# Kernel tuning notes

Measured on AMD Instinct MI355X. Metric: run time of the kernel, lower is better.

The kernel has to match this reference:

```python
import jax, jax.numpy as jnp
import numpy as np

# alpha clamp limits: balance=False -> [exp(-1/5), exp(-1/25)]
ALPHA_MIN = float(np.exp(-1.0 / 5.0))
ALPHA_MAX = float(np.exp(-1.0 / 25.0))
T_CROP = 100


def setup_inputs() -> dict:
    key = jax.random.key(0)
    k1, k2, k3 = jax.random.split(key, 3)
    B, T, D, H = 128, 1000, 1024, 256
    x = jax.random.normal(k1, (B, T, D), dtype=jnp.float32)
    bound = float(np.sqrt(1.0 / D))
    W = jax.random.uniform(k2, (H, D), minval=-bound, maxval=bound, dtype=jnp.float32)
    alpha = jax.random.uniform(k3, (H,), minval=ALPHA_MIN, maxval=ALPHA_MAX, dtype=jnp.float32)
    return {"x": x, "W": W, "alpha": alpha}


def reference(x, W, alpha):
    # x: [B, T, D], W: [H, D], alpha: [H]
    a = jnp.clip(alpha, ALPHA_MIN, ALPHA_MAX)
    Wx = jnp.einsum('btd,hd->bth', x, W)  # [B, T, H]
    T = Wx.shape[1]
    mask = (jnp.arange(T) >= T_CROP).astype(Wx.dtype)  # [T]
    Wx_t = jnp.moveaxis(Wx, 1, 0)  # [T, B, H]

    def step(carry, inp):
        ut, out = carry
        wx, m = inp
        ut = a * ut + (1.0 - a) * wx
        out = out + m * jax.nn.softmax(ut, axis=-1)
        return (ut, out), None

    B, H = Wx.shape[0], Wx.shape[2]
    init = (jnp.zeros((B, H), Wx.dtype), jnp.zeros((B, H), Wx.dtype))
    (_, out), _ = jax.lax.scan(step, init, (Wx_t, mask))
    return out  # [B, H]
```

## Files before the change

### kernel.cpp

```cpp
#include <hip/hip_runtime.h>
#include <hip/hip_bf16.h>

#define B_    128
#define T_    1000
#define D_    1024
#define H_    256
#define TCROP 100
#define CHUNK 25
#define NCHK  40
#define CSKIP 4
#define NOUTC 36

typedef __attribute__((ext_vector_type(8))) short bfrag8;
typedef __attribute__((ext_vector_type(4))) float f32x4;
typedef unsigned long long ull;

__device__ __forceinline__ float bf2f(unsigned short u) {
    union { unsigned int u; float f; } v; v.u = ((unsigned int)u) << 16;
    return v.f;
}
__device__ __forceinline__ unsigned short f2bf(float f) {
    union { float f; unsigned int u; } v; v.f = f;
    unsigned int u = v.u;
    u += 0x7FFFu + ((u >> 16) & 1u);
    return (unsigned short)(u >> 16);
}
__device__ __forceinline__ unsigned int pack2(float lo, float hi) {
    union { float f; unsigned int u; } a, b; a.f = lo; b.f = hi;
    return __builtin_amdgcn_perm(b.u + 0x8000u, a.u + 0x8000u, 0x07060302u);
}
__device__ __forceinline__ bfrag8 cvt8(float4 f0, float4 f1) {
    union { bfrag8 v; unsigned int u[4]; } r;
    r.u[0] = pack2(f0.x, f0.y);
    r.u[1] = pack2(f0.z, f0.w);
    r.u[2] = pack2(f1.x, f1.y);
    r.u[3] = pack2(f1.z, f1.w);
    return r.v;
}

__global__ __launch_bounds__(256) void wconv_kernel(
        const float* __restrict__ W, unsigned short* __restrict__ Wbf) {
    const int i = (blockIdx.x * 256 + threadIdx.x) * 8;
    float4 f0 = *(const float4*)(W + i);
    float4 f1 = *(const float4*)(W + i + 4);
    *(bfrag8*)(Wbf + i) = cvt8(f0, f1);
}

__global__ __launch_bounds__(512) void gemm_kernel(
        const float* __restrict__ x, const unsigned short* __restrict__ Wbf,
        unsigned short* __restrict__ Wx) {
    __shared__ unsigned short As[128 * 64];
    __shared__ unsigned short Bs[256 * 64];

    const int tid  = threadIdx.x;
    const int lane = tid & 63;
    const int wave = tid >> 6;
    const int wr   = wave >> 2;
    const int wc   = wave & 3;
    const int m0   = blockIdx.x * 128;

    f32x4 acc[4][4];
#pragma unroll
    for (int m = 0; m < 4; ++m)
#pragma unroll
        for (int n = 0; n < 4; ++n) acc[m][n] = (f32x4){0.f, 0.f, 0.f, 0.f};

    const int rr  = lane & 15;
    const int kh  = lane >> 4;
    const int ra0 = tid >> 3;
    const int ja  = tid & 7;
    const int sa  = (ja ^ (ra0 & 7)) * 8;
    const float* ap0 = x + (size_t)(m0 + ra0) * D_ + ja * 8;
    const float* ap1 = ap0 + (size_t)64 * D_;

    for (int it = 0; it < 16; ++it) {
        const int kt = it * 64;
        float4 f00 = *(const float4*)(ap0 + kt);
        float4 f01 = *(const float4*)(ap0 + kt + 4);
        float4 f10 = *(const float4*)(ap1 + kt);
        float4 f11 = *(const float4*)(ap1 + kt + 4);
#pragma unroll
        for (int q = 0; q < 4; ++q) {
            const int li = q * 512 + tid;
            const int r = li >> 3, j = li & 7;
            const int jj = j ^ (r & 7);
            __builtin_amdgcn_global_load_lds(
                (const __attribute__((address_space(1))) void*)
                    (Wbf + (size_t)r * D_ + kt + jj * 8),
                (__attribute__((address_space(3))) void*)&Bs[li * 8], 16, 0, 0);
        }
        *(bfrag8*)&As[ra0 * 64 + sa]        = cvt8(f00, f01);
        *(bfrag8*)&As[(ra0 + 64) * 64 + sa] = cvt8(f10, f11);
        __syncthreads();
#pragma unroll
        for (int kk = 0; kk < 2; ++kk) {
            const int c16 = kk * 4 + kh;
            bfrag8 af[4], bfr[4];
#pragma unroll
            for (int m = 0; m < 4; ++m) {
                const int row = wr * 64 + m * 16 + rr;
                af[m] = *(const bfrag8*)&As[row * 64 + ((c16 ^ (row & 7)) * 8)];
            }
#pragma unroll
            for (int n = 0; n < 4; ++n) {
                const int row = wc * 64 + n * 16 + rr;
                bfr[n] = *(const bfrag8*)&Bs[row * 64 + ((c16 ^ (row & 7)) * 8)];
            }
#pragma unroll
            for (int m = 0; m < 4; ++m)
#pragma unroll
                for (int n = 0; n < 4; ++n)
                    acc[m][n] = __builtin_amdgcn_mfma_f32_16x16x32_bf16(
                        af[m], bfr[n], acc[m][n], 0, 0, 0);
        }
        __syncthreads();
    }

    const int cl = lane & 15, rg = lane >> 4;
#pragma unroll
    for (int m = 0; m < 4; ++m)
#pragma unroll
        for (int n = 0; n < 4; ++n)
#pragma unroll
            for (int j = 0; j < 4; ++j) {
                const int row = m0 + wr * 64 + m * 16 + rg * 4 + j;
                const int col = wc * 64 + n * 16 + cl;
                Wx[(size_t)row * H_ + col] = f2bf(acc[m][n][j]);
            }
}

__global__ __launch_bounds__(256) void scanA_kernel(
        const unsigned short* __restrict__ Wx, const float* __restrict__ alpha,
        float* __restrict__ F) {
    const int wave = threadIdx.x >> 6;
    const int lane = threadIdx.x & 63;
    const int c = blockIdx.x * 4 + wave;
    const int b = blockIdx.y;
    const int h4 = lane * 4;

    const float AMIN = 0.81873075307798182f, AMAX = 0.96078943915232320f;
    float4 al = *(const float4*)(alpha + h4);
    float a[4]  = {fminf(fmaxf(al.x, AMIN), AMAX), fminf(fmaxf(al.y, AMIN), AMAX),
                   fminf(fmaxf(al.z, AMIN), AMAX), fminf(fmaxf(al.w, AMIN), AMAX)};
    float om[4] = {1.f - a[0], 1.f - a[1], 1.f - a[2], 1.f - a[3]};

    float ut[4] = {0.f, 0.f, 0.f, 0.f};
    const unsigned short* base = Wx + ((size_t)b * T_ + c * CHUNK) * H_ + h4;
#pragma unroll 5
    for (int t = 0; t < CHUNK; ++t) {
        ull wv = *(const ull*)(base + (size_t)t * H_);
        ut[0] = a[0] * ut[0] + om[0] * bf2f((unsigned short)wv);
        ut[1] = a[1] * ut[1] + om[1] * bf2f((unsigned short)(wv >> 16));
        ut[2] = a[2] * ut[2] + om[2] * bf2f((unsigned short)(wv >> 32));
        ut[3] = a[3] * ut[3] + om[3] * bf2f((unsigned short)(wv >> 48));
    }
    float4 o; o.x = ut[0]; o.y = ut[1]; o.z = ut[2]; o.w = ut[3];
    *(float4*)(F + ((size_t)b * NCHK + c) * H_ + h4) = o;
}

__global__ __launch_bounds__(256) void scanC_kernel(
        const unsigned short* __restrict__ Wx, const float* __restrict__ alpha,
        const float* __restrict__ F, float* __restrict__ P) {
    const int wave = threadIdx.x >> 6;
    const int lane = threadIdx.x & 63;
    const int c = CSKIP + blockIdx.x * 4 + wave;
    const int b = blockIdx.y;
    const int h4 = lane * 4;

    const float AMIN = 0.81873075307798182f, AMAX = 0.96078943915232320f;
    float4 al = *(const float4*)(alpha + h4);
    float a[4]  = {fminf(fmaxf(al.x, AMIN), AMAX), fminf(fmaxf(al.y, AMIN), AMAX),
                   fminf(fmaxf(al.z, AMIN), AMAX), fminf(fmaxf(al.w, AMIN), AMAX)};
    float om[4] = {1.f - a[0], 1.f - a[1], 1.f - a[2], 1.f - a[3]};

    float aL[4] = {__powf(a[0], (float)CHUNK), __powf(a[1], (float)CHUNK),
                   __powf(a[2], (float)CHUNK), __powf(a[3], (float)CHUNK)};
    float S[4] = {0.f, 0.f, 0.f, 0.f};
    for (int j = 0; j < c; ++j) {
        float4 f = *(const float4*)(F + ((size_t)b * NCHK + j) * H_ + h4);
        S[0] = aL[0] * S[0] + f.x;
        S[1] = aL[1] * S[1] + f.y;
        S[2] = aL[2] * S[2] + f.z;
        S[3] = aL[3] * S[3] + f.w;
    }

    float ut[4]   = {S[0], S[1], S[2], S[3]};
    float acc4[4] = {0.f, 0.f, 0.f, 0.f};
    const unsigned short* base = Wx + ((size_t)b * T_ + c * CHUNK) * H_ + h4;

#pragma unroll
    for (int bb = 0; bb < CHUNK; bb += 5) {
        float e[5][4], sl[5];
#pragma unroll
        for (int q = 0; q < 5; ++q) {
            ull wv = *(const ull*)(base + (size_t)(bb + q) * H_);
            ut[0] = a[0] * ut[0] + om[0] * bf2f((unsigned short)wv);
            ut[1] = a[1] * ut[1] + om[1] * bf2f((unsigned short)(wv >> 16));
            ut[2] = a[2] * ut[2] + om[2] * bf2f((unsigned short)(wv >> 32));
            ut[3] = a[3] * ut[3] + om[3] * bf2f((unsigned short)(wv >> 48));
            e[q][0] = __expf(ut[0]);
            e[q][1] = __expf(ut[1]);
            e[q][2] = __expf(ut[2]);
            e[q][3] = __expf(ut[3]);
            sl[q] = (e[q][0] + e[q][1]) + (e[q][2] + e[q][3]);
        }
#pragma unroll
        for (int dd = 1; dd < 64; dd <<= 1) {
            sl[0] += __shfl_xor(sl[0], dd);
            sl[1] += __shfl_xor(sl[1], dd);
            sl[2] += __shfl_xor(sl[2], dd);
            sl[3] += __shfl_xor(sl[3], dd);
            sl[4] += __shfl_xor(sl[4], dd);
        }
#pragma unroll
        for (int q = 0; q < 5; ++q) {
            const float rcp = 1.0f / sl[q];
            acc4[0] += e[q][0] * rcp;
            acc4[1] += e[q][1] * rcp;
            acc4[2] += e[q][2] * rcp;
            acc4[3] += e[q][3] * rcp;
        }
    }
    float4 o; o.x = acc4[0]; o.y = acc4[1]; o.z = acc4[2]; o.w = acc4[3];
    *(float4*)(P + ((size_t)b * NOUTC + (c - CSKIP)) * H_ + h4) = o;
}

__global__ __launch_bounds__(256) void scanD_kernel(
        const float* __restrict__ P, float* __restrict__ out) {
    const int b = blockIdx.x, h = threadIdx.x;
    float s = 0.f;
#pragma unroll 4
    for (int k = 0; k < NOUTC; ++k) s += P[((size_t)b * NOUTC + k) * H_ + h];
    out[(size_t)b * H_ + h] = s;
}

extern "C" void kernel_launch(void* const* d_in, const int* in_sizes, int n_in,
                              void* d_out, int out_size, void* d_ws, size_t ws_size,
                              hipStream_t stream) {
    const float* x     = (const float*)d_in[0];
    const float* W     = (const float*)d_in[1];
    const float* alpha = (const float*)d_in[2];
    float* out = (float*)d_out;

    char* ws = (char*)d_ws;
    unsigned short* Wbf = (unsigned short*)ws;
    unsigned short* Wx  = (unsigned short*)(ws + ((size_t)1 << 20));
    float* F = (float*)(ws + ((size_t)70 << 20));
    float* P = (float*)(ws + ((size_t)80 << 20));

    wconv_kernel<<<128, 256, 0, stream>>>(W, Wbf);
    gemm_kernel<<<(B_ * T_) / 128, 512, 0, stream>>>(x, Wbf, Wx);
    scanA_kernel<<<dim3(NCHK / 4, B_), 256, 0, stream>>>(Wx, alpha, F);
    scanC_kernel<<<dim3(NOUTC / 4, B_), 256, 0, stream>>>(Wx, alpha, F, P);
    scanD_kernel<<<B_, 256, 0, stream>>>(P, out);
}
```

Baseline: 188.2 us.

## Fuse chunk-local EMA scan into GEMM epilogue via LDS-staged tile

The GEMM now tiles by 125 time steps per batch element, so each block holds 5 whole scan chunks. The output tile is staged in swizzled shared memory. Half the threads compute the per-chunk EMA partial sums F from LDS, and the other half write Wx to global with 16-byte stores. This removes the separate scanA kernel and its re-read of Wx, and skips writing Wx rows before the crop offset, which scanC does not need. In exchange the MMA tiles run partly wasted (125 of 128 rows), the epilogue is longer and serial, and the tail x rows are clamped duplicate loads.

Result: no change. 187.3 us (-0.5%).

```diff
diff --git a/kernel.cpp b/kernel.cpp
--- a/kernel.cpp
+++ b/kernel.cpp
@@ -10,6 +10,7 @@
 #define NCHK  40
 #define CSKIP 4
 #define NOUTC 36
+#define BM    125
 
 typedef __attribute__((ext_vector_type(8))) short bfrag8;
 typedef __attribute__((ext_vector_type(4))) float f32x4;
@@ -46,18 +47,22 @@
     *(bfrag8*)(Wbf + i) = cvt8(f0, f1);
 }
 
-__global__ __launch_bounds__(512) void gemm_kernel(
+__global__ __launch_bounds__(512) void gemm_ema_kernel(
         const float* __restrict__ x, const unsigned short* __restrict__ Wbf,
-        unsigned short* __restrict__ Wx) {
-    __shared__ unsigned short As[128 * 64];
-    __shared__ unsigned short Bs[256 * 64];
+        const float* __restrict__ alpha,
+        unsigned short* __restrict__ Wx, float* __restrict__ F) {
+    __shared__ unsigned short smem[32000];
+    unsigned short* As = smem;
+    unsigned short* Bs = smem + 128 * 64;
 
     const int tid  = threadIdx.x;
     const int lane = tid & 63;
     const int wave = tid >> 6;
     const int wr   = wave >> 2;
     const int wc   = wave & 3;
-    const int m0   = blockIdx.x * 128;
+    const int c    = blockIdx.x;
+    const int b    = blockIdx.y;
+    const int m0   = b * T_ + c * BM;
 
     f32x4 acc[4][4];
 #pragma unroll
@@ -70,8 +75,9 @@
     const int ra0 = tid >> 3;
     const int ja  = tid & 7;
     const int sa  = (ja ^ (ra0 & 7)) * 8;
+    const int r1  = (ra0 + 64 <= BM - 1) ? ra0 + 64 : BM - 1;
     const float* ap0 = x + (size_t)(m0 + ra0) * D_ + ja * 8;
-    const float* ap1 = ap0 + (size_t)64 * D_;
+    const float* ap1 = x + (size_t)(m0 + r1) * D_ + ja * 8;
 
     for (int it = 0; it < 16; ++it) {
         const int kt = it * 64;
@@ -123,39 +129,43 @@
         for (int n = 0; n < 4; ++n)
 #pragma unroll
             for (int j = 0; j < 4; ++j) {
-                const int row = m0 + wr * 64 + m * 16 + rg * 4 + j;
-                const int col = wc * 64 + n * 16 + cl;
-                Wx[(size_t)row * H_ + col] = f2bf(acc[m][n][j]);
-            }
-}
-
-__global__ __launch_bounds__(256) void scanA_kernel(
-        const unsigned short* __restrict__ Wx, const float* __restrict__ alpha,
-        float* __restrict__ F) {
-    const int wave = threadIdx.x >> 6;
-    const int lane = threadIdx.x & 63;
-    const int c = blockIdx.x * 4 + wave;
-    const int b = blockIdx.y;
-    const int h4 = lane * 4;
-
-    const float AMIN = 0.81873075307798182f, AMAX = 0.96078943915232320f;
-    float4 al = *(const float4*)(alpha + h4);
-    float a[4]  = {fminf(fmaxf(al.x, AMIN), AMAX), fminf(fmaxf(al.y, AMIN), AMAX),
-                   fminf(fmaxf(al.z, AMIN), AMAX), fminf(fmaxf(al.w, AMIN), AMAX)};
-    float om[4] = {1.f - a[0], 1.f - a[1], 1.f - a[2], 1.f - a[3]};
-
-    float ut[4] = {0.f, 0.f, 0.f, 0.f};
-    const unsigned short* base = Wx + ((size_t)b * T_ + c * CHUNK) * H_ + h4;
+                const int row = wr * 64 + m * 16 + rg * 4 + j;
+                if (row < BM) {
+                    const int col = wc * 64 + n * 16 + cl;
+                    smem[row * 256 + (col ^ (((row >> 2) & 3) << 4))] =
+                        f2bf(acc[m][n][j]);
+                }
+            }
+    __syncthreads();
+
+    if (tid < 256) {
+        const int h = tid;
+        const float AMIN = 0.81873075307798182f, AMAX = 0.96078943915232320f;
+        const float a  = fminf(fmaxf(alpha[h], AMIN), AMAX);
+        const float om = 1.0f - a;
+        float ut = 0.f;
+        const size_t fbase = ((size_t)b * NCHK + c * 5) * H_ + h;
 #pragma unroll 5
-    for (int t = 0; t < CHUNK; ++t) {
-        ull wv = *(const ull*)(base + (size_t)t * H_);
-        ut[0] = a[0] * ut[0] + om[0] * bf2f((unsigned short)wv);
-        ut[1] = a[1] * ut[1] + om[1] * bf2f((unsigned short)(wv >> 16));
-        ut[2] = a[2] * ut[2] + om[2] * bf2f((unsigned short)(wv >> 32));
-        ut[3] = a[3] * ut[3] + om[3] * bf2f((unsigned short)(wv >> 48));
-    }
-    float4 o; o.x = ut[0]; o.y = ut[1]; o.z = ut[2]; o.w = ut[3];
-    *(float4*)(F + ((size_t)b * NCHK + c) * H_ + h4) = o;
+        for (int r = 0; r < BM; ++r) {
+            ut = a * ut + om * bf2f(smem[r * 256 + (h ^ (((r >> 2) & 3) << 4))]);
+            if ((r % 25) == 24) {
+                F[fbase + (size_t)(r / 25) * H_] = ut;
+                ut = 0.f;
+            }
+        }
+    } else {
+        const int nrows = (c == 0) ? (BM - TCROP) : BM;
+        const int rbase = (c == 0) ? TCROP : 0;
+        const int total = nrows * 32;
+        for (int li = tid - 256; li < total; li += 256) {
+            const int r  = rbase + (li >> 5);
+            const int cg = (li & 31) * 8;
+            const int scg = cg ^ (((r >> 2) & 3) << 4);
+            bfrag8 v = *(const bfrag8*)&smem[r * 256 + scg];
+            const int t = c * BM + r;
+            *(bfrag8*)&Wx[((size_t)b * T_ + t) * H_ + cg] = v;
+        }
+    }
 }
 
 __global__ __launch_bounds__(256) void scanC_kernel(
@@ -249,8 +259,7 @@
     float* P = (float*)(ws + ((size_t)80 << 20));
 
     wconv_kernel<<<128, 256, 0, stream>>>(W, Wbf);
-    gemm_kernel<<<(B_ * T_) / 128, 512, 0, stream>>>(x, Wbf, Wx);
-    scanA_kernel<<<dim3(NCHK / 4, B_), 256, 0, stream>>>(Wx, alpha, F);
+    gemm_ema_kernel<<<dim3(T_ / BM, B_), 512, 0, stream>>>(x, Wbf, alpha, Wx, F);
     scanC_kernel<<<dim3(NOUTC / 4, B_), 256, 0, stream>>>(Wx, alpha, F, P);
     scanD_kernel<<<B_, 256, 0, stream>>>(P, out);
 }
```
